# Kernel optimization log

Measured on AMD Instinct MI355X. Metric: run time of the kernel, lower is better.

Reference implementation:

```python
import jax, jax.numpy as jnp
import numpy as np

MODES = 16

def _spectral_conv(x, w1r, w1i, w2r, w2i):
    # x: [N, Cin, R, R]; weights: [Cin, Cout, MODES, MODES] (real/imag parts)
    N, Cin, R, _ = x.shape
    Cout = w1r.shape[1]
    x_ft = jnp.fft.rfft2(x, axes=(-2, -1))  # [N, Cin, R, R//2+1] complex
    w1 = w1r + 1j * w1i
    w2 = w2r + 1j * w2i
    top = jnp.einsum('ncxy,coxy->noxy', x_ft[:, :, :MODES, :MODES], w1)
    bot = jnp.einsum('ncxy,coxy->noxy', x_ft[:, :, -MODES:, :MODES], w2)
    out_ft = jnp.zeros((N, Cout, R, R // 2 + 1), dtype=x_ft.dtype)
    out_ft = out_ft.at[:, :, :MODES, :MODES].set(top)
    out_ft = out_ft.at[:, :, -MODES:, :MODES].set(bot)
    return jnp.fft.irfft2(out_ft, s=(R, R), axes=(-2, -1))

def _forward(ref, w1r, w1i, w2r, w2i, subdomain_lookup):
    B, S, C, R, _ = ref.shape
    x = ref.reshape(B * S, C, R, R)
    # spectral conv + residual for ALL subdomains at once (vectorizes the torch loop)
    u_sub = _spectral_conv(x, w1r, w1i, w2r, w2i) + x  # [B*S, C, R, R]
    flat = u_sub.reshape(B, S, C, R * R)
    idx = subdomain_lookup.reshape(-1)  # [R*R], values in [0, S)
    pos = jnp.arange(R * R)
    # per-pixel select of owning subdomain: u[b, c, p] = flat[b, idx[p], c, p]
    # advanced indices (idx, pos) separated by a slice move to the front -> [R*R, B, C]
    u = flat[:, idx, :, pos]
    return jnp.transpose(u, (1, 2, 0)).reshape(B, C, R, R)

def setup_inputs():
    key = jax.random.key(0)
    ks = jax.random.split(key, 7)
    B, S, C, R, M = 4, 16, 64, 128, MODES
    scale = 1.0 / (C * C)
    return {
        'reference': jax.random.normal(ks[0], (B, S, C, R, R), dtype=jnp.float32),
        'physical_coords': jax.random.normal(ks[1], (2, R, R), dtype=jnp.float32),
        'subdomain_lookup': jax.random.randint(ks[2], (R, R), 0, S),
        'w1r': scale * jax.random.normal(ks[3], (C, C, M, M), dtype=jnp.float32),
        'w1i': scale * jax.random.normal(ks[4], (C, C, M, M), dtype=jnp.float32),
        'w2r': scale * jax.random.normal(ks[5], (C, C, M, M), dtype=jnp.float32),
        'w2i': scale * jax.random.normal(ks[6], (C, C, M, M), dtype=jnp.float32),
    }

def reference(reference, physical_coords, subdomain_lookup, w1r, w1i, w2r, w2i):
    del physical_coords  # only used for shape checks / dead ref_grid in the original
    return _forward(reference, w1r, w1i, w2r, w2i, subdomain_lookup)
```

## Files before the change

### kernel.cpp

```cpp
#include <hip/hip_runtime.h>
#include <math.h>


#define TWO_PI_OVER_128 0.04908738521234052f
#define RCAP 1280

typedef __attribute__((ext_vector_type(8))) short bf16x8;
typedef __attribute__((ext_vector_type(4))) float f32x4;
union FragU { uint4 u; bf16x8 s; };

__device__ __forceinline__ unsigned pk(float a, float b) {
  unsigned ua = __float_as_uint(a), ub = __float_as_uint(b);
  ua = (ua + 0x7FFFu + ((ua >> 16) & 1u)) >> 16;
  ub = (ub + 0x7FFFu + ((ub >> 16) & 1u)) >> 16;
  return ua | (ub << 16);
}
__device__ __forceinline__ float2 upk(unsigned v) {
  return make_float2(__uint_as_float(v << 16), __uint_as_float(v & 0xFFFF0000u));
}
__device__ __forceinline__ unsigned bf1(float a) {
  unsigned ua = __float_as_uint(a);
  return (ua + 0x7FFFu + ((ua >> 16) & 1u)) >> 16;
}

__global__ __launch_bounds__(1024) void kprep(const int* __restrict__ lu,
                                              int* __restrict__ scomb,
                                              int* __restrict__ plist,
                                              int* __restrict__ cntg,
                                              int* __restrict__ cnthg,
                                              unsigned* __restrict__ Etu,
                                              unsigned* __restrict__ Gtu,
                                              unsigned* __restrict__ G2tu,
                                              const float* __restrict__ w1r,
                                              const float* __restrict__ w1i,
                                              const float* __restrict__ w2r,
                                              const float* __restrict__ w2i,
                                              unsigned* __restrict__ Wt) {
  __shared__ int wsum[16];
  __shared__ unsigned tile[64 * 65];
  const int blk = blockIdx.x;
  const int tid = threadIdx.x;
  if (blk < 16) {
    const int s = blk;
    const int lane = tid & 63, wid = tid >> 6;
    const int4* lu4 = (const int4*)lu + tid * 4;
    unsigned match = 0;
#pragma unroll
    for (int q = 0; q < 4; ++q) {
      int4 v = lu4[q];
      match |= (v.x == s ? 1u : 0u) << (4 * q);
      match |= (v.y == s ? 1u : 0u) << (4 * q + 1);
      match |= (v.z == s ? 1u : 0u) << (4 * q + 2);
      match |= (v.w == s ? 1u : 0u) << (4 * q + 3);
    }
    const int cnt = __popc(match);
    int pre = cnt;
#pragma unroll
    for (int d = 1; d < 64; d <<= 1) {
      int t = __shfl_up(pre, d, 64);
      if (lane >= d) pre += t;
    }
    if (lane == 63) wsum[wid] = pre;
    __syncthreads();
    int woff = 0;
    for (int j = 0; j < wid; ++j) woff += wsum[j];
    int r = woff + pre - cnt;
    if (tid == 512) cnthg[s] = r;
    const int base = tid * 16;
#pragma unroll
    for (int i = 0; i < 16; ++i) {
      if ((match >> i) & 1u) {
        const int p = base + i;
        scomb[p] = (s << 12) | r;
        if (r < RCAP) plist[s * RCAP + r] = p;
        ++r;
      }
    }
    if (tid == 1023) {
      const int tot = woff + pre;
      cntg[s] = (tot < RCAP) ? tot : RCAP;
    }
  } else if (blk == 16) {
    for (int i = 0; i < 2; ++i) {
      int t = i * 1024 + tid;
      int w = t >> 6, y0 = (t & 63) * 2;
      float v[2];
#pragma unroll
      for (int q = 0; q < 2; ++q) {
        int y = y0 + q;
        if (w < 16) v[q] = cosf((float)((w * y) & 127) * TWO_PI_OVER_128);
        else        v[q] = -sinf((float)(((w - 16) * y) & 127) * TWO_PI_OVER_128);
      }
      Etu[t] = bf1(v[0]) | (bf1(v[1]) << 16);
    }
    for (int i = 0; i < 4; ++i) {
      int t = i * 1024 + tid;
      int jr = t >> 6, x0 = (t & 63) * 2;
      int j = (jr & 31);
      int kx = (j < 16) ? j : 96 + j;
      float v[2];
#pragma unroll
      for (int q = 0; q < 2; ++q) {
        int x = x0 + q;
        float a = (float)((kx * x) & 127) * TWO_PI_OVER_128;
        v[q] = (jr < 32) ? cosf(a) : sinf(a);
      }
      Gtu[t] = bf1(v[0]) | (bf1(v[1]) << 16);
    }
    for (int i = 0; i < 4; ++i) {
      int t = i * 1024 + tid;
      int x = t >> 5, k2 = t & 31;
      float v[2];
#pragma unroll
      for (int q = 0; q < 2; ++q) {
        int k = k2 * 2 + q;
        int kxi = k & 31;
        int kxe = (kxi < 16) ? kxi : 96 + kxi;
        float a = (float)((kxe * x) & 127) * TWO_PI_OVER_128;
        v[q] = (k < 32) ? cosf(a) : sinf(a);
      }
      G2tu[t] = bf1(v[0]) | (bf1(v[1]) << 16);
    }
  } else {
    const int ob = blk - 17;
    const int o = ob & 63, wsel = ob >> 6;
    const float* Wr = wsel ? w2r : w1r;
    const float* Wi = wsel ? w2i : w1i;
    for (int mc = 0; mc < 4; ++mc) {
      if (mc) __syncthreads();
      for (int i = 0; i < 4; ++i) {
        int idx = i * 1024 + tid;
        int c = idx >> 6, ml = idx & 63;
        int mh = mc * 64 + ml;
        float wsc = ((mh & 15) ? 2.f : 1.f) / 16384.f;
        size_t off = (size_t)(c * 64 + o) * 256 + mh;
        tile[c * 65 + ml] = pk(Wr[off] * wsc, Wi[off] * wsc);
      }
      __syncthreads();
      for (int i = 0; i < 4; ++i) {
        int idx = i * 1024 + tid;
        int ml = idx >> 6, c = idx & 63;
        Wt[(size_t)(wsel * 256 + mc * 64 + ml) * 4096 + o * 64 + c] = tile[c * 65 + ml];
      }
    }
  }
}

__global__ __launch_bounds__(256, 4) void k1_fwd(const float* __restrict__ ref,
                                                 const unsigned* __restrict__ Etu,
                                                 const unsigned* __restrict__ Gtu,
                                                 const int* __restrict__ cntg,
                                                 const int* __restrict__ cnthg,
                                                 const int* __restrict__ plist,
                                                 unsigned short* __restrict__ Rcomp,
                                                 unsigned* __restrict__ Xf) {
  __shared__ unsigned short imgL[64 * 128];
  __shared__ unsigned short A1t[2][32 * 128];
  unsigned* Xout = (unsigned*)imgL;
  const int bid2 = blockIdx.x;
  const int n = bid2 >> 5, cp = bid2 & 31;
  const int c0 = cp * 2;
  const int b = n >> 4, s = n & 15;
  const int tid = threadIdx.x;
  const int l = tid & 63, w = tid >> 6;

  FragU Ef[2][4];
#pragma unroll
  for (int nt = 0; nt < 2; ++nt)
#pragma unroll
    for (int ks = 0; ks < 4; ++ks)
      Ef[nt][ks].u = *(const uint4*)&Etu[(nt * 16 + (l & 15)) * 64 + ks * 16 + (l >> 4) * 4];

  const int ns = cntg[s], nh = cnthg[s];
  const int* pl = plist + s * RCAP;

  for (int img = 0; img < 2; ++img) {
    const int c = c0 + img;
    const float* imf = ref + (size_t)((n << 6) + c) * 16384;
    unsigned short* rc = Rcomp + ((size_t)((b << 6) + c) * 16 + s) * RCAP;
    for (int half = 0; half < 2; ++half) {
      if (img | half) __syncthreads();
      const float4* im4 = (const float4*)(imf + half * 8192);
      for (int i = 0; i < 8; ++i) {
        const int e4 = i * 256 + tid;
        float4 v = im4[e4];
        const int pl2 = e4 * 4;
        const int xl = pl2 >> 7, y0 = pl2 & 127;
        const int chunk = (y0 >> 3) ^ (xl & 15);
        *(uint2*)&imgL[xl * 128 + chunk * 8 + (y0 & 7)] =
            make_uint2(pk(v.x, v.y), pk(v.z, v.w));
      }
      __syncthreads();
      f32x4 acc1[2] = {};
      const int xl = w * 16 + (l & 15);
#pragma unroll
      for (int ks = 0; ks < 4; ++ks) {
        const int chunk = (ks * 4 + (l >> 4)) ^ (xl & 15);
        FragU a;
        a.u = *(const uint4*)&imgL[xl * 128 + chunk * 8];
#pragma unroll
        for (int nt = 0; nt < 2; ++nt)
          acc1[nt] = __builtin_amdgcn_mfma_f32_16x16x32_bf16(a.s, Ef[nt][ks].s, acc1[nt], 0, 0, 0);
      }
      {
        const int x0 = (half * 4 + w) * 16 + (l >> 4) * 4;
#pragma unroll
        for (int nt = 0; nt < 2; ++nt) {
          const int wp = nt * 16 + (l & 15);
          const int chunk = (x0 >> 3) ^ (wp & 15);
          *(uint2*)&A1t[img][wp * 128 + chunk * 8 + (x0 & 7)] =
              make_uint2(pk(acc1[nt][0], acc1[nt][1]), pk(acc1[nt][2], acc1[nt][3]));
        }
      }
      {
        const int rlo = half ? nh : 0, rhi = half ? ns : nh;
        for (int r = rlo + tid; r < rhi; r += 256) {
          const int p = pl[r];
          const int gxl = (p >> 7) - half * 64, y = p & 127;
          rc[r] = imgL[gxl * 128 + (((y >> 3) ^ (gxl & 15))) * 8 + (y & 7)];
        }
      }
    }
  }
  __syncthreads();

  {
    const int wi = w >> 1, wl = w & 1;
    FragU Gf[2];
    f32x4 acc2[2][2] = {};
#pragma unroll
    for (int ks = 0; ks < 4; ++ks) {
#pragma unroll
      for (int mtl = 0; mtl < 2; ++mtl)
        Gf[mtl].u = *(const uint4*)&Gtu[((wl + 2 * mtl) * 16 + (l & 15)) * 64 + ks * 16 + (l >> 4) * 4];
#pragma unroll
      for (int nt = 0; nt < 2; ++nt) {
        const int wp = nt * 16 + (l & 15);
        const int chunk = (ks * 4 + (l >> 4)) ^ (wp & 15);
        FragU bfr;
        bfr.u = *(const uint4*)&A1t[wi][wp * 128 + chunk * 8];
#pragma unroll
        for (int mtl = 0; mtl < 2; ++mtl)
          acc2[mtl][nt] = __builtin_amdgcn_mfma_f32_16x16x32_bf16(Gf[mtl].s, bfr.s, acc2[mtl][nt], 0, 0, 0);
      }
    }
#pragma unroll
    for (int r = 0; r < 4; ++r) {
      const int j = wl * 16 + (l >> 4) * 4 + r;
      const int ky = l & 15;
      const float re = acc2[0][0][r] + acc2[1][1][r];
      const float im = acc2[0][1][r] - acc2[1][0][r];
      Xout[wi * 512 + j * 16 + ky] = pk(re, im);
    }
  }
  __syncthreads();
  {
    uint2* dst = (uint2*)(Xf + (size_t)((n << 6) + c0) * 512);
    const uint2* src = (const uint2*)Xout;
    dst[tid] = src[tid];
    dst[tid + 256] = src[tid + 256];
  }
}

__global__ __launch_bounds__(256) void kt(const unsigned* __restrict__ Xf,
                                          unsigned* __restrict__ Xf2) {
  __shared__ unsigned tile[64 * 65];
  const int bm = blockIdx.x & 7, bn = blockIdx.x >> 3;
  const int tid = threadIdx.x;
  for (int i = 0; i < 16; ++i) {
    int idx = i * 256 + tid;
    int r = idx >> 6, cc = idx & 63;
    tile[r * 65 + cc] = Xf[(size_t)(bn * 64 + r) * 512 + bm * 64 + cc];
  }
  __syncthreads();
  for (int i = 0; i < 16; ++i) {
    int idx = i * 256 + tid;
    int r = idx >> 6, cc = idx & 63;
    Xf2[(size_t)(bm * 64 + r) * 4096 + bn * 64 + cc] = tile[cc * 65 + r];
  }
}

__global__ __launch_bounds__(256) void k2_mix(const unsigned* __restrict__ Xf2,
                                              const unsigned* __restrict__ Wt,
                                              unsigned* __restrict__ Yf) {
  __shared__ unsigned short Xr[64 * 64];
  __shared__ unsigned short Xi[64 * 64];
  __shared__ unsigned short Wr[64 * 64];
  __shared__ unsigned short Wi[64 * 64];
  const int m = blockIdx.x;
  const int tid = threadIdx.x;
  const int l = tid & 63, w = tid >> 6;
  for (int i = 0; i < 8; ++i) {
    const int e0 = (i * 256 + tid) * 2;
    const int n = e0 >> 6, cc = e0 & 63;
    const int pos = n * 64 + (((cc >> 3) ^ (n & 7)) << 3) + (cc & 7);
    uint2 xv = *(const uint2*)&Xf2[(size_t)m * 4096 + e0];
    *(unsigned*)&Xr[pos] = (xv.x & 0xFFFFu) | (xv.y << 16);
    *(unsigned*)&Xi[pos] = (xv.x >> 16) | (xv.y & 0xFFFF0000u);
    uint2 wv = *(const uint2*)&Wt[(size_t)m * 4096 + e0];
    *(unsigned*)&Wr[pos] = (wv.x & 0xFFFFu) | (wv.y << 16);
    *(unsigned*)&Wi[pos] = (wv.x >> 16) | (wv.y & 0xFFFF0000u);
  }
  __syncthreads();
  f32x4 acc[4][4] = {};
  const int arow = w * 16 + (l & 15);
#pragma unroll
  for (int ks = 0; ks < 2; ++ks) {
    FragU Ar, Ai;
    {
      const int chunk = ((ks * 4 + (l >> 4))) ^ (arow & 7);
      Ar.u = *(const uint4*)&Xr[arow * 64 + chunk * 8];
      Ai.u = *(const uint4*)&Xi[arow * 64 + chunk * 8];
    }
#pragma unroll
    for (int nt = 0; nt < 4; ++nt) {
      const int orow = nt * 16 + (l & 15);
      const int chunk = ((ks * 4 + (l >> 4))) ^ (orow & 7);
      FragU Br, Bi;
      Br.u = *(const uint4*)&Wr[orow * 64 + chunk * 8];
      Bi.u = *(const uint4*)&Wi[orow * 64 + chunk * 8];
      acc[nt][0] = __builtin_amdgcn_mfma_f32_16x16x32_bf16(Ar.s, Br.s, acc[nt][0], 0, 0, 0);
      acc[nt][1] = __builtin_amdgcn_mfma_f32_16x16x32_bf16(Ai.s, Bi.s, acc[nt][1], 0, 0, 0);
      acc[nt][2] = __builtin_amdgcn_mfma_f32_16x16x32_bf16(Ar.s, Bi.s, acc[nt][2], 0, 0, 0);
      acc[nt][3] = __builtin_amdgcn_mfma_f32_16x16x32_bf16(Ai.s, Br.s, acc[nt][3], 0, 0, 0);
    }
  }
#pragma unroll
  for (int nt = 0; nt < 4; ++nt) {
    unsigned o4[4];
#pragma unroll
    for (int r = 0; r < 4; ++r)
      o4[r] = pk(acc[nt][0][r] - acc[nt][1][r], acc[nt][2][r] + acc[nt][3][r]);
    const int bo = w * 64 + nt * 16 + (l & 15);
    *(uint4*)&Yf[(size_t)bo * 8192 + m * 16 + (l >> 4) * 4] = *(uint4*)o4;
  }
}

__global__ __launch_bounds__(1024, 4) void k3_inv(const unsigned* __restrict__ Yf,
                                                  const unsigned* __restrict__ G2tu,
                                                  const int* __restrict__ scomb,
                                                  const unsigned short* __restrict__ Rcomp,
                                                  float* __restrict__ out) {
  __shared__ __align__(16) unsigned short Ypb[16 * 32 * 40];
  __shared__ __align__(16) unsigned short tbuf[16 * 546];
  __shared__ float2 tab[128];
  const int bo = blockIdx.x >> 1, half = blockIdx.x & 1;
  const int tid = threadIdx.x;
  const int l = tid & 63, w = tid >> 6;
  if (tid < 128) {
    float sv, cv;
    sincosf((float)tid * TWO_PI_OVER_128, &sv, &cv);
    tab[tid] = make_float2(cv, sv);
  }
  {
    const unsigned* src = Yf + (size_t)bo * 8192;
    for (int i = 0; i < 8; ++i) {
      int e = i * 1024 + tid;
      unsigned v = src[e];
      int ss = e & 15, m = e >> 4, kxi = m >> 4, ky = m & 15;
      unsigned short* yb = Ypb + ss * 1280;
      yb[ky * 40 + kxi] = (unsigned short)(v & 0xFFFFu);
      yb[(16 + ky) * 40 + kxi] = (unsigned short)(v >> 16);
    }
  }
  __syncthreads();
  float* outb = out + (size_t)bo * 16384;
  const unsigned short* rcb = Rcomp + (size_t)bo * 16 * RCAP;
  unsigned* tb32 = (unsigned*)tbuf;

  for (int ch = 0; ch < 4; ++ch) {
    const int xb = half * 64 + ch * 16;
    {
      const int xg = xb + (l & 15);
      FragU Ac, As, B0, B1;
      Ac.u = *(const uint4*)&G2tu[xg * 32 + (l >> 4) * 4];
      As.u = *(const uint4*)&G2tu[xg * 32 + 16 + (l >> 4) * 4];
      const unsigned short* yb = Ypb + w * 1280;
      B0.u = *(const uint4*)&yb[(l & 15) * 40 + (l >> 4) * 8];
      B1.u = *(const uint4*)&yb[(16 + (l & 15)) * 40 + (l >> 4) * 8];
      f32x4 z = {};
      f32x4 d1  = __builtin_amdgcn_mfma_f32_16x16x32_bf16(Ac.s, B0.s, z, 0, 0, 0);
      f32x4 d1b = __builtin_amdgcn_mfma_f32_16x16x32_bf16(Ac.s, B1.s, z, 0, 0, 0);
      f32x4 d2  = __builtin_amdgcn_mfma_f32_16x16x32_bf16(As.s, B0.s, z, 0, 0, 0);
      f32x4 d2b = __builtin_amdgcn_mfma_f32_16x16x32_bf16(As.s, B1.s, z, 0, 0, 0);
      const int ky = l & 15;
#pragma unroll
      for (int r = 0; r < 4; ++r) {
        const int xloc = (l >> 4) * 4 + r;
        tb32[w * 273 + xloc * 17 + ky] = pk(d1[r] - d2b[r], d1b[r] + d2[r]);
      }
    }
    __syncthreads();
    {
      const int xg = xb + w;
      const int pbase = xg * 128 + l * 2;
      const int2 sc2 = *(const int2*)&scomb[pbase];
      float o2[2];
#pragma unroll
      for (int q = 0; q < 2; ++q) {
        const int y = l * 2 + q;
        const int sc = q ? sc2.y : sc2.x;
        const int ssel = sc >> 12;
        const float rres = __uint_as_float((unsigned)rcb[ssel * RCAP + (sc & 4095)] << 16);
        const unsigned* tb = tb32 + ssel * 273 + w * 17;
        const float2 stpy = tab[y];
        float acc = 0.f, c0 = 1.f, s0 = 0.f;
#pragma unroll
        for (int k2 = 0; k2 < 16; ++k2) {
          const float2 tt = upk(tb[k2]);
          acc = fmaf(tt.x, c0, fmaf(-tt.y, s0, acc));
          float nc = c0 * stpy.x - s0 * stpy.y, ns = s0 * stpy.x + c0 * stpy.y;
          c0 = nc; s0 = ns;
        }
        o2[q] = rres + acc;
      }
      *(float2*)&outb[pbase] = make_float2(o2[0], o2[1]);
    }
    __syncthreads();
  }
}

extern "C" void kernel_launch(void* const* d_in, const int* in_sizes, int n_in,
                              void* d_out, int out_size, void* d_ws, size_t ws_size,
                              hipStream_t stream) {
  const float* ref = (const float*)d_in[0];
  const int* lu = (const int*)d_in[2];
  const float* w1r = (const float*)d_in[3];
  const float* w1i = (const float*)d_in[4];
  const float* w2r = (const float*)d_in[5];
  const float* w2i = (const float*)d_in[6];
  float* out = (float*)d_out;

  unsigned* Xf  = (unsigned*)d_ws;
  unsigned* Xf2 = Xf  + (size_t)4096 * 512;
  unsigned* Wt  = Xf2 + (size_t)4096 * 512;
  unsigned* Etu = Wt  + (size_t)4096 * 512;
  unsigned* Gtu = Etu + 2048;
  unsigned* G2tu = Gtu + 4096;
  int* cntg     = (int*)(G2tu + 4096);
  int* cnthg    = cntg + 16;
  int* plist    = cnthg + 16;
  int* scomb    = plist + 16 * RCAP;
  unsigned short* Rcomp = (unsigned short*)(scomb + 16384);
  unsigned* Yf  = Xf;

  kprep<<<145, 1024, 0, stream>>>(lu, scomb, plist, cntg, cnthg,
                                  Etu, Gtu, G2tu, w1r, w1i, w2r, w2i, Wt);
  k1_fwd<<<2048, 256, 0, stream>>>(ref, Etu, Gtu, cntg, cnthg, plist, Rcomp, Xf);
  kt<<<512, 256, 0, stream>>>(Xf, Xf2);
  k2_mix<<<512, 256, 0, stream>>>(Xf2, Wt, Yf);
  k3_inv<<<512, 1024, 0, stream>>>(Yf, G2tu, scomb, Rcomp, out);
}
```

Before: 113.1 us.

## Register-prefetch next image half and share twiddle recurrence across paired output columns

```diff
diff --git a/kernel.cpp b/kernel.cpp
--- a/kernel.cpp
+++ b/kernel.cpp
@@ -173,52 +173,61 @@
 
   const int ns = cntg[s], nh = cnthg[s];
   const int* pl = plist + s * RCAP;
-
-  for (int img = 0; img < 2; ++img) {
-    const int c = c0 + img;
-    const float* imf = ref + (size_t)((n << 6) + c) * 16384;
-    unsigned short* rc = Rcomp + ((size_t)((b << 6) + c) * 16 + s) * RCAP;
-    for (int half = 0; half < 2; ++half) {
-      if (img | half) __syncthreads();
-      const float4* im4 = (const float4*)(imf + half * 8192);
-      for (int i = 0; i < 8; ++i) {
-        const int e4 = i * 256 + tid;
-        float4 v = im4[e4];
-        const int pl2 = e4 * 4;
-        const int xl = pl2 >> 7, y0 = pl2 & 127;
-        const int chunk = (y0 >> 3) ^ (xl & 15);
-        *(uint2*)&imgL[xl * 128 + chunk * 8 + (y0 & 7)] =
-            make_uint2(pk(v.x, v.y), pk(v.z, v.w));
-      }
-      __syncthreads();
-      f32x4 acc1[2] = {};
-      const int xl = w * 16 + (l & 15);
-#pragma unroll
-      for (int ks = 0; ks < 4; ++ks) {
-        const int chunk = (ks * 4 + (l >> 4)) ^ (xl & 15);
-        FragU a;
-        a.u = *(const uint4*)&imgL[xl * 128 + chunk * 8];
-#pragma unroll
-        for (int nt = 0; nt < 2; ++nt)
-          acc1[nt] = __builtin_amdgcn_mfma_f32_16x16x32_bf16(a.s, Ef[nt][ks].s, acc1[nt], 0, 0, 0);
-      }
-      {
-        const int x0 = (half * 4 + w) * 16 + (l >> 4) * 4;
-#pragma unroll
-        for (int nt = 0; nt < 2; ++nt) {
-          const int wp = nt * 16 + (l & 15);
-          const int chunk = (x0 >> 3) ^ (wp & 15);
-          *(uint2*)&A1t[img][wp * 128 + chunk * 8 + (x0 & 7)] =
-              make_uint2(pk(acc1[nt][0], acc1[nt][1]), pk(acc1[nt][2], acc1[nt][3]));
-        }
-      }
-      {
-        const int rlo = half ? nh : 0, rhi = half ? ns : nh;
-        for (int r = rlo + tid; r < rhi; r += 256) {
-          const int p = pl[r];
-          const int gxl = (p >> 7) - half * 64, y = p & 127;
-          rc[r] = imgL[gxl * 128 + (((y >> 3) ^ (gxl & 15))) * 8 + (y & 7)];
-        }
+  const float* imf0 = ref + (size_t)((n << 6) + c0) * 16384;
+
+  float4 v[8];
+  {
+    const float4* p = (const float4*)imf0;
+#pragma unroll
+    for (int i = 0; i < 8; ++i) v[i] = p[i * 256 + tid];
+  }
+
+  for (int st = 0; st < 4; ++st) {
+    const int img = st >> 1, half = st & 1;
+    if (st) __syncthreads();
+#pragma unroll
+    for (int i = 0; i < 8; ++i) {
+      const int pl2 = (i * 256 + tid) * 4;
+      const int xl = pl2 >> 7, y0 = pl2 & 127;
+      const int chunk = (y0 >> 3) ^ (xl & 15);
+      *(uint2*)&imgL[xl * 128 + chunk * 8 + (y0 & 7)] =
+          make_uint2(pk(v[i].x, v[i].y), pk(v[i].z, v[i].w));
+    }
+    __syncthreads();
+    if (st < 3) {
+      const int st2 = st + 1;
+      const float4* p = (const float4*)(imf0 + (st2 >> 1) * 16384 + (st2 & 1) * 8192);
+#pragma unroll
+      for (int i = 0; i < 8; ++i) v[i] = p[i * 256 + tid];
+    }
+    f32x4 acc1[2] = {};
+    const int xl = w * 16 + (l & 15);
+#pragma unroll
+    for (int ks = 0; ks < 4; ++ks) {
+      const int chunk = (ks * 4 + (l >> 4)) ^ (xl & 15);
+      FragU a;
+      a.u = *(const uint4*)&imgL[xl * 128 + chunk * 8];
+#pragma unroll
+      for (int nt = 0; nt < 2; ++nt)
+        acc1[nt] = __builtin_amdgcn_mfma_f32_16x16x32_bf16(a.s, Ef[nt][ks].s, acc1[nt], 0, 0, 0);
+    }
+    {
+      const int x0 = (half * 4 + w) * 16 + (l >> 4) * 4;
+#pragma unroll
+      for (int nt = 0; nt < 2; ++nt) {
+        const int wp = nt * 16 + (l & 15);
+        const int chunk = (x0 >> 3) ^ (wp & 15);
+        *(uint2*)&A1t[img][wp * 128 + chunk * 8 + (x0 & 7)] =
+            make_uint2(pk(acc1[nt][0], acc1[nt][1]), pk(acc1[nt][2], acc1[nt][3]));
+      }
+    }
+    {
+      unsigned short* rc = Rcomp + ((size_t)((b << 6) + c0 + img) * 16 + s) * RCAP;
+      const int rlo = half ? nh : 0, rhi = half ? ns : nh;
+      for (int r = rlo + tid; r < rhi; r += 256) {
+        const int p = pl[r];
+        const int gxl = (p >> 7) - half * 64, y = p & 127;
+        rc[r] = imgL[gxl * 128 + (((y >> 3) ^ (gxl & 15))) * 8 + (y & 7)];
       }
     }
   }
@@ -393,28 +402,28 @@
     __syncthreads();
     {
       const int xg = xb + w;
-      const int pbase = xg * 128 + l * 2;
-      const int2 sc2 = *(const int2*)&scomb[pbase];
-      float o2[2];
-#pragma unroll
-      for (int q = 0; q < 2; ++q) {
-        const int y = l * 2 + q;
-        const int sc = q ? sc2.y : sc2.x;
-        const int ssel = sc >> 12;
-        const float rres = __uint_as_float((unsigned)rcb[ssel * RCAP + (sc & 4095)] << 16);
-        const unsigned* tb = tb32 + ssel * 273 + w * 17;
-        const float2 stpy = tab[y];
-        float acc = 0.f, c0 = 1.f, s0 = 0.f;
-#pragma unroll
-        for (int k2 = 0; k2 < 16; ++k2) {
-          const float2 tt = upk(tb[k2]);
-          acc = fmaf(tt.x, c0, fmaf(-tt.y, s0, acc));
-          float nc = c0 * stpy.x - s0 * stpy.y, ns = s0 * stpy.x + c0 * stpy.y;
-          c0 = nc; s0 = ns;
-        }
-        o2[q] = rres + acc;
-      }
-      *(float2*)&outb[pbase] = make_float2(o2[0], o2[1]);
+      const int p0 = xg * 128 + l;
+      const int sc0 = scomb[p0], sc1 = scomb[p0 + 64];
+      const int ssa = sc0 >> 12, ssb = sc1 >> 12;
+      const float r0 = __uint_as_float((unsigned)rcb[ssa * RCAP + (sc0 & 4095)] << 16);
+      const float r1 = __uint_as_float((unsigned)rcb[ssb * RCAP + (sc1 & 4095)] << 16);
+      const unsigned* tb0 = tb32 + ssa * 273 + w * 17;
+      const unsigned* tb1 = tb32 + ssb * 273 + w * 17;
+      const float2 stpy = tab[l];
+      float acc0 = 0.f, acc1e = 0.f, acc1o = 0.f;
+      float c0 = 1.f, s0 = 0.f;
+#pragma unroll
+      for (int k2 = 0; k2 < 16; ++k2) {
+        const float2 ta = upk(tb0[k2]);
+        const float2 tc = upk(tb1[k2]);
+        acc0 = fmaf(ta.x, c0, fmaf(-ta.y, s0, acc0));
+        if (k2 & 1) acc1o = fmaf(tc.x, c0, fmaf(-tc.y, s0, acc1o));
+        else        acc1e = fmaf(tc.x, c0, fmaf(-tc.y, s0, acc1e));
+        float nc = c0 * stpy.x - s0 * stpy.y, ns = s0 * stpy.x + c0 * stpy.y;
+        c0 = nc; s0 = ns;
+      }
+      outb[p0] = r0 + acc0;
+      outb[p0 + 64] = r1 + (acc1e - acc1o);
     }
     __syncthreads();
   }
```

Result: no change. 113.1 us, median of 2 (+0.1%).
